# Optimization experiments

Hardware: AMD Instinct MI355X
Metric: run time of the kernel (lower is better)

Reference implementation:

```python
import jax, jax.numpy as jnp
import numpy as np

H = 16          # num query heads
G = 4           # num kv heads (groups)
MAX_POS = 128   # max relative position


def setup_inputs() -> dict:
    key = jax.random.key(0)
    ks = jax.random.split(key, 6)
    B, T, D = 8, 1024, 1024
    hd = D // H
    s = 0.02
    return {
        "x": jax.random.normal(ks[0], (B, T, D), jnp.float32),
        "Wq": jax.random.normal(ks[1], (D, D), jnp.float32) * s,
        "Wk": jax.random.normal(ks[2], (hd * G, D), jnp.float32) * s,
        "Wv": jax.random.normal(ks[3], (hd * G, D), jnp.float32) * s,
        "Wo": jax.random.normal(ks[4], (D, D), jnp.float32) * s,
        "E": jax.random.normal(ks[5], (2 * MAX_POS - 1, hd), jnp.float32) * s,
    }


def reference(x, Wq, Wk, Wv, Wo, E):
    B, T, D = x.shape
    hd = D // H
    r = H // G  # kv repeat factor

    # projections (torch nn.Linear convention: y = x @ W.T)
    q = (x @ Wq.T).reshape(B, T, H, hd).transpose(0, 2, 1, 3)  # [B,H,T,hd]
    k = (x @ Wk.T).reshape(B, T, G, hd)                         # [B,T,G,hd]
    v = (x @ Wv.T).reshape(B, T, G, hd)

    # GQA: query head h uses kv group h // r  (matches repeat_interleave)
    k = jnp.repeat(k, r, axis=2).transpose(0, 2, 1, 3)  # [B,H,T,hd]
    v = jnp.repeat(v, r, axis=2).transpose(0, 2, 1, 3)  # [B,H,T,hd]

    q = q * (1.0 / hd) ** 0.5
    scores = jnp.einsum("bhqd,bhkd->bhqk", q, k)  # [B,H,T,T]

    # relative position bias: R[i,j] = E[clamp(j - i) + MAX_POS - 1]
    pos = jnp.arange(T)
    dist = jnp.clip(pos[None, :] - pos[:, None], -MAX_POS + 1, MAX_POS - 1) + MAX_POS - 1
    R = E[dist]  # [T,T,hd]
    # original einsum 'bhd,thd->bht' with q=[B*H, Tq, hd], R=[Tk, Tq, hd]:
    # bias[b,h,q,kpos] = sum_d q[b,h,q,d] * R[kpos, q, d]
    bias = jnp.einsum("bhqd,kqd->bhqk", q, R)
    scores = scores + bias

    attn = jax.nn.softmax(scores, axis=-1)
    out = jnp.einsum("bhqk,bhkd->bhqd", attn, v)         # [B,H,T,hd]
    out = out.transpose(0, 2, 1, 3).reshape(B, T, D)      # [B,T,D]
    return out @ Wo.T
```

## Files before the change

### kernel.cpp

```cpp
#include <hip/hip_runtime.h>
#include <hip/hip_bf16.h>
#include <cstdint>
#include <cstddef>

typedef __hip_bfloat16 bf16;
typedef __attribute__((ext_vector_type(8))) __bf16 bf16x8;
typedef __attribute__((ext_vector_type(4))) float floatx4;

#define GPTR(p) ((const __attribute__((address_space(1))) void*)(p))
#define LPTR(p) ((__attribute__((address_space(3))) void*)(p))

extern "C" __device__ float __ocml_native_exp2_f32(float);
__device__ __forceinline__ float exp2n(float x) {
  return __ocml_native_exp2_f32(x);
}

__device__ __forceinline__ floatx4 mfma16(bf16x8 a, bf16x8 b, floatx4 c) {
  return __builtin_amdgcn_mfma_f32_16x16x32_bf16(a, b, c, 0, 0, 0);
}

__global__ __launch_bounds__(256) void cvt_bf16(const float* __restrict__ in,
                                                bf16* __restrict__ out, int n4) {
  for (int i = blockIdx.x * 256 + threadIdx.x; i < n4; i += gridDim.x * 256) {
    float4 v = ((const float4*)in)[i];
    alignas(8) bf16 t[4] = {__float2bfloat16(v.x), __float2bfloat16(v.y),
                            __float2bfloat16(v.z), __float2bfloat16(v.w)};
    *(uint64_t*)(out + (size_t)i * 4) = *(const uint64_t*)t;
  }
}

__global__ __launch_bounds__(256) void cvt_w3(const float* __restrict__ wq,
                                              const float* __restrict__ wk,
                                              const float* __restrict__ wv,
                                              bf16* __restrict__ oq,
                                              bf16* __restrict__ ok,
                                              bf16* __restrict__ ov) {
  int i = blockIdx.x * 256 + threadIdx.x;
  const float* in;
  bf16* out;
  int j;
  if (i < 262144) {
    in = wq; out = oq; j = i;
  } else if (i < 327680) {
    in = wk; out = ok; j = i - 262144;
  } else {
    in = wv; out = ov; j = i - 327680;
  }
  float4 v = ((const float4*)in)[j];
  alignas(8) bf16 t[4] = {__float2bfloat16(v.x), __float2bfloat16(v.y),
                          __float2bfloat16(v.z), __float2bfloat16(v.w)};
  *(uint64_t*)(out + (size_t)j * 4) = *(const uint64_t*)t;
}

__device__ __forceinline__ void stage128_swz(const bf16* __restrict__ g,
                                             int gstride,
                                             bf16* __restrict__ dst, int tid) {
#pragma unroll
  for (int s = 0; s < 4; ++s) {
    int f = s * 256 + tid;
    int r = f >> 3, cb = f & 7;
    int cbg = cb ^ (r & 7);
    __builtin_amdgcn_global_load_lds(GPTR(g + (size_t)r * gstride + cbg * 8),
                                     LPTR(dst + f * 8), 16, 0, 0);
  }
}

__device__ __forceinline__ bf16x8 rd128_swz(const bf16* __restrict__ tile,
                                            int row, int ci) {
  return *(const bf16x8*)&tile[row * 64 + ((ci ^ (row & 7)) * 8)];
}

__global__ __launch_bounds__(256) void gemm_qkv(
    const bf16* __restrict__ A, const bf16* __restrict__ Wq,
    const bf16* __restrict__ Wk, const bf16* __restrict__ Wv,
    bf16* __restrict__ qout, bf16* __restrict__ kout,
    bf16* __restrict__ vTout) {
  __shared__ alignas(16) bf16 As[128 * 64];
  __shared__ alignas(16) bf16 Bs[128 * 64];
  const int tid = threadIdx.x;
  const int lane = tid & 63;
  const int w = tid >> 6;
  const int wr = w >> 1, wc = w & 1;
  const int quad = lane >> 4, c = lane & 15;
  const int phys = blockIdx.y * 12 + blockIdx.x;
  const int ll = phys >> 3;
  const int m0 = ((phys & 7) * 8 + ll / 12) * 128;
  const int nb = ll % 12;

  int mode, nloc;
  const bf16* Wp;
  if (nb < 8) {
    mode = 1; Wp = Wq + (size_t)nb * 128 * 1024; nloc = nb * 128;
  } else if (nb < 10) {
    mode = 2; Wp = Wk + (size_t)(nb - 8) * 128 * 1024; nloc = (nb - 8) * 128;
  } else {
    mode = 3; Wp = Wv + (size_t)(nb - 10) * 128 * 1024; nloc = (nb - 10) * 128;
  }

  const bf16* pa = A + (size_t)m0 * 1024;
  const bf16* pb = Wp;

  floatx4 acc[4][4] = {};

  for (int kt = 0; kt < 16; ++kt) {
    if (kt) __syncthreads();
    stage128_swz(pa, 1024, As, tid);
    stage128_swz(pb, 1024, Bs, tid);
    pa += 64; pb += 64;
    __syncthreads();
#pragma unroll
    for (int kk = 0; kk < 2; ++kk) {
      bf16x8 af[4], bfr[4];
#pragma unroll
      for (int i = 0; i < 4; ++i)
        af[i] = rd128_swz(As, wr * 64 + i * 16 + c, kk * 4 + quad);
#pragma unroll
      for (int j = 0; j < 4; ++j)
        bfr[j] = rd128_swz(Bs, wc * 64 + j * 16 + c, kk * 4 + quad);
#pragma unroll
      for (int i = 0; i < 4; ++i)
#pragma unroll
        for (int j = 0; j < 4; ++j)
          acc[i][j] = mfma16(af[i], bfr[j], acc[i][j]);
    }
  }

  if (mode == 3) {
#pragma unroll
    for (int i = 0; i < 4; ++i)
#pragma unroll
      for (int j = 0; j < 4; ++j) {
        int m = m0 + wr * 64 + i * 16 + quad * 4;
        int n = nloc + wc * 64 + j * 16 + c;
        int b = m >> 10, t = m & 1023, g = n >> 6, d = n & 63;
        alignas(8) bf16 tmp[4];
#pragma unroll
        for (int r = 0; r < 4; ++r) tmp[r] = __float2bfloat16(acc[i][j][r]);
        *(uint64_t*)(vTout + (((size_t)(b * 4 + g)) * 64 + d) * 1024 + t) =
            *(const uint64_t*)tmp;
      }
    return;
  }

  const float scale = (mode == 1) ? 0.18033688f : 1.0f;
#pragma unroll
  for (int i = 0; i < 4; ++i)
#pragma unroll
    for (int j = 0; j < 4; ++j)
#pragma unroll
      for (int r = 0; r < 4; ++r) {
        int m = m0 + wr * 64 + i * 16 + quad * 4 + r;
        int n = nloc + wc * 64 + j * 16 + c;
        int b = m >> 10, t = m & 1023;
        bf16 v = __float2bfloat16(acc[i][j][r] * scale);
        if (mode == 1) {
          int h = n >> 6;
          qout[(((size_t)(b * 16 + h)) * 1024 + t) * 64 + (n & 63)] = v;
        } else {
          int g = n >> 6;
          kout[(((size_t)(b * 4 + g)) * 1024 + t) * 64 + (n & 63)] = v;
        }
      }
}

__global__ __launch_bounds__(256) void gemm_o(const bf16* __restrict__ A,
                                              const bf16* __restrict__ W,
                                              float* __restrict__ out) {
  __shared__ alignas(16) bf16 As[128 * 64];
  __shared__ alignas(16) bf16 Bs[128 * 64];
  const int tid = threadIdx.x;
  const int lane = tid & 63;
  const int w = tid >> 6;
  const int wr = w >> 1, wc = w & 1;
  const int quad = lane >> 4, c = lane & 15;
  const int phys = blockIdx.y * 8 + blockIdx.x;
  const int ll = phys >> 3;
  const int m0 = ((phys & 7) * 8 + (ll >> 3)) * 128;
  const int n0 = (ll & 7) * 128;

  const bf16* pa = A + (size_t)m0 * 1024;
  const bf16* pb = W + (size_t)n0 * 1024;

  floatx4 acc[4][4] = {};

  for (int kt = 0; kt < 16; ++kt) {
    if (kt) __syncthreads();
    stage128_swz(pa, 1024, As, tid);
    stage128_swz(pb, 1024, Bs, tid);
    pa += 64; pb += 64;
    __syncthreads();
#pragma unroll
    for (int kk = 0; kk < 2; ++kk) {
      bf16x8 af[4], bfr[4];
#pragma unroll
      for (int i = 0; i < 4; ++i)
        af[i] = rd128_swz(As, wr * 64 + i * 16 + c, kk * 4 + quad);
#pragma unroll
      for (int j = 0; j < 4; ++j)
        bfr[j] = rd128_swz(Bs, wc * 64 + j * 16 + c, kk * 4 + quad);
#pragma unroll
      for (int i = 0; i < 4; ++i)
#pragma unroll
        for (int j = 0; j < 4; ++j)
          acc[i][j] = mfma16(af[i], bfr[j], acc[i][j]);
    }
  }

#pragma unroll
  for (int i = 0; i < 4; ++i)
#pragma unroll
    for (int j = 0; j < 4; ++j)
#pragma unroll
      for (int r = 0; r < 4; ++r) {
        int m = m0 + wr * 64 + i * 16 + quad * 4 + r;
        int n = n0 + wc * 64 + j * 16 + c;
        out[(size_t)m * 1024 + n] = acc[i][j][r];
      }
}

__device__ __forceinline__ void stage_tile_swz(const bf16* __restrict__ g,
                                               int gstride, bf16* __restrict__ dst,
                                               int tid) {
#pragma unroll
  for (int s = 0; s < 2; ++s) {
    int f = s * 256 + tid;
    int r = f >> 3, cb = f & 7;
    int cbg = cb ^ (r & 7);
    __builtin_amdgcn_global_load_lds(GPTR(g + (size_t)r * gstride + cbg * 8),
                                     LPTR(dst + f * 8), 16, 0, 0);
  }
}

__device__ __forceinline__ bf16x8 read_frag_swz(const bf16* __restrict__ tile,
                                                int row, int cb) {
  return *(const bf16x8*)&tile[row * 64 + ((cb ^ (row & 7)) * 8)];
}

__global__ __launch_bounds__(256, 3) void attn_kernel(
    const bf16* __restrict__ q_ws, const bf16* __restrict__ k_ws,
    const bf16* __restrict__ vT, const float* __restrict__ E,
    bf16* __restrict__ out) {
  __shared__ alignas(16) bf16 qEl[64 * 264];
  __shared__ alignas(16) bf16 Ks[64 * 72];
  __shared__ alignas(16) bf16 Vs[64 * 64];
  const int tid = threadIdx.x;
  const int lane = tid & 63, w = tid >> 6;
  const int quad = lane >> 4, c = lane & 15;
  const int phys = blockIdx.y * 16 + blockIdx.x;
  const int logical = (phys & 7) * 256 + (phys >> 3);
  const int bh = logical >> 4;
  const int b = bh >> 4, h = bh & 15, g = h >> 2;
  const int qb = (logical & 15) * 64 + w * 16;

  const bf16* qrow = q_ws + ((size_t)bh * 1024 + qb + c) * 64;
  bf16x8 qf0 = *(const bf16x8*)(qrow + quad * 8);
  bf16x8 qf1 = *(const bf16x8*)(qrow + 32 + quad * 8);

  for (int jn = 0; jn < 16; ++jn) {
    int er = jn * 16 + c;
    er = er > 254 ? 254 : er;
    const float* Ep = E + (size_t)er * 64;
    float4 e0 = *(const float4*)(Ep + quad * 8);
    float4 e1 = *(const float4*)(Ep + quad * 8 + 4);
    float4 e2 = *(const float4*)(Ep + 32 + quad * 8);
    float4 e3 = *(const float4*)(Ep + 32 + quad * 8 + 4);
    alignas(16) bf16 t0b[8] = {
        __float2bfloat16(e0.x), __float2bfloat16(e0.y), __float2bfloat16(e0.z),
        __float2bfloat16(e0.w), __float2bfloat16(e1.x), __float2bfloat16(e1.y),
        __float2bfloat16(e1.z), __float2bfloat16(e1.w)};
    alignas(16) bf16 t1b[8] = {
        __float2bfloat16(e2.x), __float2bfloat16(e2.y), __float2bfloat16(e2.z),
        __float2bfloat16(e2.w), __float2bfloat16(e3.x), __float2bfloat16(e3.y),
        __float2bfloat16(e3.z), __float2bfloat16(e3.w)};
    floatx4 a = {};
    a = mfma16(qf0, *(const bf16x8*)t0b, a);
    a = mfma16(qf1, *(const bf16x8*)t1b, a);
#pragma unroll
    for (int r = 0; r < 4; ++r)
      qEl[(w * 16 + quad * 4 + r) * 264 + jn * 16 + c] = __float2bfloat16(a[r]);
  }
  __syncthreads();

  const bf16* rowE = qEl + (size_t)(w * 16 + c) * 264;
  bf16* rowP = Ks + (size_t)(w * 16 + c) * 72;
  float mrow = -1e30f, lpart = 0.f;
  floatx4 o[4] = {};
  const bf16* kbase = k_ws + (size_t)(b * 4 + g) * 1024 * 64;
  const bf16* vbase = vT + (size_t)(b * 4 + g) * 64 * 1024;
  const float blo = __bfloat162float(rowE[254]);
  const float bhi = __bfloat162float(rowE[0]);

  for (int t0 = 0; t0 < 1024; t0 += 64) {
    stage_tile_swz(kbase + (size_t)t0 * 64, 64, Ks, tid);
    stage_tile_swz(vbase + t0, 1024, Vs, tid);
    __syncthreads();
    floatx4 S[4];
#pragma unroll
    for (int j = 0; j < 4; ++j) {
      bf16x8 kf0 = read_frag_swz(Ks, j * 16 + c, quad);
      bf16x8 kf1 = read_frag_swz(Ks, j * 16 + c, quad + 4);
      floatx4 z = {};
      z = mfma16(kf0, qf0, z);
      S[j] = mfma16(kf1, qf1, z);
    }
    const int dlt0 = qb + c - t0;
    if (t0 <= qb - 190) {
#pragma unroll
      for (int j = 0; j < 4; ++j)
#pragma unroll
        for (int r = 0; r < 4; ++r) S[j][r] += blo;
    } else if (t0 >= qb + 142) {
#pragma unroll
      for (int j = 0; j < 4; ++j)
#pragma unroll
        for (int r = 0; r < 4; ++r) S[j][r] += bhi;
    } else {
#pragma unroll
      for (int j = 0; j < 4; ++j)
#pragma unroll
        for (int r = 0; r < 4; ++r) {
          int dlt = dlt0 - j * 16 - quad * 4 - r;
          dlt = dlt > 127 ? 127 : (dlt < -127 ? -127 : dlt);
          S[j][r] += __bfloat162float(rowE[dlt + 127]);
        }
    }
    float mx = S[0][0];
#pragma unroll
    for (int j = 0; j < 4; ++j)
#pragma unroll
      for (int r = 0; r < 4; ++r) mx = fmaxf(mx, S[j][r]);
    if (__ballot(mx > mrow + 11.5f)) {
      float fm = fmaxf(mx, __shfl_xor(mx, 16, 64));
      fm = fmaxf(fm, __shfl_xor(fm, 32, 64));
      float nm = fmaxf(mrow, fm);
      float alpha = exp2n(mrow - nm);
      float av[4];
#pragma unroll
      for (int r = 0; r < 4; ++r) av[r] = __shfl(alpha, quad * 4 + r, 64);
#pragma unroll
      for (int jj = 0; jj < 4; ++jj)
#pragma unroll
        for (int r = 0; r < 4; ++r) o[jj][r] *= av[r];
      lpart *= alpha;
      mrow = nm;
    }
    float rs = 0.f;
#pragma unroll
    for (int j = 0; j < 4; ++j)
#pragma unroll
      for (int r = 0; r < 4; ++r) {
        float p = exp2n(S[j][r] - mrow);
        S[j][r] = p;
        rs += p;
      }
    lpart += rs;
    __syncthreads();
#pragma unroll
    for (int j = 0; j < 4; ++j) {
      alignas(8) bf16 tmp[4];
#pragma unroll
      for (int r = 0; r < 4; ++r) tmp[r] = __float2bfloat16(S[j][r]);
      *(uint64_t*)(rowP + j * 16 + quad * 4) = *(const uint64_t*)tmp;
    }
    __threadfence_block();
    __builtin_amdgcn_wave_barrier();
    bf16x8 pf0 = *(const bf16x8*)(rowP + quad * 8);
    bf16x8 pf1 = *(const bf16x8*)(rowP + 32 + quad * 8);
#pragma unroll
    for (int jj = 0; jj < 4; ++jj) {
      bf16x8 vf0 = read_frag_swz(Vs, jj * 16 + c, quad);
      bf16x8 vf1 = read_frag_swz(Vs, jj * 16 + c, quad + 4);
      o[jj] = mfma16(pf0, vf0, o[jj]);
      o[jj] = mfma16(pf1, vf1, o[jj]);
    }
    __syncthreads();
  }

  float lsum = lpart + __shfl_xor(lpart, 16, 64);
  lsum += __shfl_xor(lsum, 32, 64);
  float lr4[4];
#pragma unroll
  for (int r = 0; r < 4; ++r) lr4[r] = __shfl(lsum, quad * 4 + r, 64);
#pragma unroll
  for (int jj = 0; jj < 4; ++jj)
#pragma unroll
    for (int r = 0; r < 4; ++r) {
      int qi = qb + quad * 4 + r;
      out[(((size_t)b * 1024 + qi) * 16 + h) * 64 + jj * 16 + c] =
          __float2bfloat16(o[jj][r] / lr4[r]);
    }
}

extern "C" void kernel_launch(void* const* d_in, const int* in_sizes, int n_in,
                              void* d_out, int out_size, void* d_ws,
                              size_t ws_size, hipStream_t stream) {
  const float* x = (const float*)d_in[0];
  const float* Wq = (const float*)d_in[1];
  const float* Wk = (const float*)d_in[2];
  const float* Wv = (const float*)d_in[3];
  const float* Wo = (const float*)d_in[4];
  const float* E = (const float*)d_in[5];

  char* ws = (char*)d_ws;
  bf16* q_ws = (bf16*)d_out;
  bf16* x_bf = (bf16*)((char*)d_out + (16ull << 20));
  bf16* k_ws = (bf16*)(ws);
  bf16* vT = (bf16*)(ws + (4ull << 20));
  bf16* attn = (bf16*)(ws + (8ull << 20));
  bf16* Wq_bf = (bf16*)(ws + (8ull << 20));
  bf16* Wk_bf = (bf16*)(ws + (10ull << 20));
  bf16* Wv_bf = (bf16*)(ws + (10ull << 20) + (512ull << 10));
  bf16* Wo_bf = (bf16*)(ws);
  float* outp = (float*)d_out;

  cvt_bf16<<<2048, 256, 0, stream>>>(x, x_bf, 2097152);
  cvt_w3<<<1536, 256, 0, stream>>>(Wq, Wk, Wv, Wq_bf, Wk_bf, Wv_bf);
  gemm_qkv<<<dim3(12, 64), 256, 0, stream>>>(x_bf, Wq_bf, Wk_bf, Wv_bf,
                                             q_ws, k_ws, vT);
  attn_kernel<<<dim3(16, 128), 256, 0, stream>>>(q_ws, k_ws, vT, E, attn);
  cvt_bf16<<<1024, 256, 0, stream>>>(Wo, Wo_bf, 262144);
  gemm_o<<<dim3(8, 64), 256, 0, stream>>>(attn, Wo_bf, outp);
}
```

Before: 268.3 us.

## Merge conversion kernels into one launch and raise wave priority around MFMA

The separate fp32-to-bf16 conversion kernels for x, Wq/Wk/Wv and Wo are combined into a single launch. When the workspace is large enough, Wo is converted early into its own region, which removes one launch and the gap between launches. In the attention kernel, s_setprio is raised around the QK and PV MFMA blocks, and the final per-element division is replaced by a reciprocal multiply. The priority change may or may not help scheduling, and the Wo path depends on ws_size.

Result: faster. 261.9 us (median of 2 runs) (-2.4%).

```diff
diff --git a/kernel.cpp b/kernel.cpp
--- a/kernel.cpp
+++ b/kernel.cpp
@@ -19,37 +19,43 @@
   return __builtin_amdgcn_mfma_f32_16x16x32_bf16(a, b, c, 0, 0, 0);
 }
 
+__device__ __forceinline__ void cvt4(const float* __restrict__ in,
+                                     bf16* __restrict__ out, int i) {
+  float4 v = ((const float4*)in)[i];
+  alignas(8) bf16 t[4] = {__float2bfloat16(v.x), __float2bfloat16(v.y),
+                          __float2bfloat16(v.z), __float2bfloat16(v.w)};
+  *(uint64_t*)(out + (size_t)i * 4) = *(const uint64_t*)t;
+}
+
 __global__ __launch_bounds__(256) void cvt_bf16(const float* __restrict__ in,
                                                 bf16* __restrict__ out, int n4) {
   for (int i = blockIdx.x * 256 + threadIdx.x; i < n4; i += gridDim.x * 256) {
-    float4 v = ((const float4*)in)[i];
-    alignas(8) bf16 t[4] = {__float2bfloat16(v.x), __float2bfloat16(v.y),
-                            __float2bfloat16(v.z), __float2bfloat16(v.w)};
-    *(uint64_t*)(out + (size_t)i * 4) = *(const uint64_t*)t;
-  }
-}
-
-__global__ __launch_bounds__(256) void cvt_w3(const float* __restrict__ wq,
-                                              const float* __restrict__ wk,
-                                              const float* __restrict__ wv,
-                                              bf16* __restrict__ oq,
-                                              bf16* __restrict__ ok,
-                                              bf16* __restrict__ ov) {
-  int i = blockIdx.x * 256 + threadIdx.x;
-  const float* in;
-  bf16* out;
-  int j;
-  if (i < 262144) {
-    in = wq; out = oq; j = i;
-  } else if (i < 327680) {
-    in = wk; out = ok; j = i - 262144;
+    cvt4(in, out, i);
+  }
+}
+
+__global__ __launch_bounds__(256) void cvt_all(
+    const float* __restrict__ x, const float* __restrict__ wq,
+    const float* __restrict__ wk, const float* __restrict__ wv,
+    const float* __restrict__ wo, bf16* __restrict__ ox,
+    bf16* __restrict__ oq, bf16* __restrict__ ok, bf16* __restrict__ ov,
+    bf16* __restrict__ owo) {
+  const int bid = blockIdx.x;
+  if (bid < 2048) {
+    for (int i = bid * 256 + threadIdx.x; i < 2097152; i += 2048 * 256)
+      cvt4(x, ox, i);
+  } else if (bid < 3584) {
+    int i = (bid - 2048) * 256 + threadIdx.x;
+    if (i < 262144) {
+      cvt4(wq, oq, i);
+    } else if (i < 327680) {
+      cvt4(wk, ok, i - 262144);
+    } else {
+      cvt4(wv, ov, i - 327680);
+    }
   } else {
-    in = wv; out = ov; j = i - 327680;
-  }
-  float4 v = ((const float4*)in)[j];
-  alignas(8) bf16 t[4] = {__float2bfloat16(v.x), __float2bfloat16(v.y),
-                          __float2bfloat16(v.z), __float2bfloat16(v.w)};
-  *(uint64_t*)(out + (size_t)j * 4) = *(const uint64_t*)t;
+    cvt4(wo, owo, (bid - 3584) * 256 + threadIdx.x);
+  }
 }
 
 __device__ __forceinline__ void stage128_swz(const bf16* __restrict__ g,
@@ -295,6 +301,7 @@
     stage_tile_swz(vbase + t0, 1024, Vs, tid);
     __syncthreads();
     floatx4 S[4];
+    __builtin_amdgcn_s_setprio(1);
 #pragma unroll
     for (int j = 0; j < 4; ++j) {
       bf16x8 kf0 = read_frag_swz(Ks, j * 16 + c, quad);
@@ -303,6 +310,7 @@
       z = mfma16(kf0, qf0, z);
       S[j] = mfma16(kf1, qf1, z);
     }
+    __builtin_amdgcn_s_setprio(0);
     const int dlt0 = qb + c - t0;
     if (t0 <= qb - 190) {
 #pragma unroll
@@ -366,6 +374,7 @@
     __builtin_amdgcn_wave_barrier();
     bf16x8 pf0 = *(const bf16x8*)(rowP + quad * 8);
     bf16x8 pf1 = *(const bf16x8*)(rowP + 32 + quad * 8);
+    __builtin_amdgcn_s_setprio(1);
 #pragma unroll
     for (int jj = 0; jj < 4; ++jj) {
       bf16x8 vf0 = read_frag_swz(Vs, jj * 16 + c, quad);
@@ -373,21 +382,23 @@
       o[jj] = mfma16(pf0, vf0, o[jj]);
       o[jj] = mfma16(pf1, vf1, o[jj]);
     }
+    __builtin_amdgcn_s_setprio(0);
     __syncthreads();
   }
 
   float lsum = lpart + __shfl_xor(lpart, 16, 64);
   lsum += __shfl_xor(lsum, 32, 64);
-  float lr4[4];
-#pragma unroll
-  for (int r = 0; r < 4; ++r) lr4[r] = __shfl(lsum, quad * 4 + r, 64);
+  float linv = 1.0f / lsum;
+  float li4[4];
+#pragma unroll
+  for (int r = 0; r < 4; ++r) li4[r] = __shfl(linv, quad * 4 + r, 64);
 #pragma unroll
   for (int jj = 0; jj < 4; ++jj)
 #pragma unroll
     for (int r = 0; r < 4; ++r) {
       int qi = qb + quad * 4 + r;
       out[(((size_t)b * 1024 + qi) * 16 + h) * 64 + jj * 16 + c] =
-          __float2bfloat16(o[jj][r] / lr4[r]);
+          __float2bfloat16(o[jj][r] * li4[r]);
     }
 }
 
@@ -410,14 +421,16 @@
   bf16* Wq_bf = (bf16*)(ws + (8ull << 20));
   bf16* Wk_bf = (bf16*)(ws + (10ull << 20));
   bf16* Wv_bf = (bf16*)(ws + (10ull << 20) + (512ull << 10));
-  bf16* Wo_bf = (bf16*)(ws);
   float* outp = (float*)d_out;
 
-  cvt_bf16<<<2048, 256, 0, stream>>>(x, x_bf, 2097152);
-  cvt_w3<<<1536, 256, 0, stream>>>(Wq, Wk, Wv, Wq_bf, Wk_bf, Wv_bf);
+  const bool early_wo = ws_size >= (26ull << 20);
+  bf16* Wo_bf = early_wo ? (bf16*)(ws + (24ull << 20)) : (bf16*)ws;
+
+  cvt_all<<<early_wo ? 4608 : 3584, 256, 0, stream>>>(
+      x, Wq, Wk, Wv, Wo, x_bf, Wq_bf, Wk_bf, Wv_bf, Wo_bf);
   gemm_qkv<<<dim3(12, 64), 256, 0, stream>>>(x_bf, Wq_bf, Wk_bf, Wv_bf,
                                              q_ws, k_ws, vT);
   attn_kernel<<<dim3(16, 128), 256, 0, stream>>>(q_ws, k_ws, vT, E, attn);
-  cvt_bf16<<<1024, 256, 0, stream>>>(Wo, Wo_bf, 262144);
+  if (!early_wo) cvt_bf16<<<1024, 256, 0, stream>>>(Wo, Wo_bf, 262144);
   gemm_o<<<dim3(8, 64), 256, 0, stream>>>(attn, Wo_bf, outp);
 }
```
